# Performance work log

Measured on AMD Instinct MI355X. Metric: run time of the kernel, lower is better.

## Reference

```python
import jax, jax.numpy as jnp
import numpy as np

B, L, D, H, FF = 2, 2048, 1024, 16, 4096
DH = D // H
EPS = 1e-5  # torch LayerNorm default


def _layernorm(x, g, b):
    mu = jnp.mean(x, axis=-1, keepdims=True)
    var = jnp.mean(jnp.square(x - mu), axis=-1, keepdims=True)
    return (x - mu) * jax.lax.rsqrt(var + EPS) * g + b


def setup_inputs() -> dict:
    key = jax.random.key(0)
    ks = jax.random.split(key, 8)
    s = 0.02  # typical init scale for weights
    return {
        "x": jax.random.normal(ks[0], (B, L, D), jnp.float32),
        "pos_embed": jax.random.normal(ks[1], (1, L, D), jnp.float32) * s,
        "ln1_g": jnp.ones((D,), jnp.float32),
        "ln1_b": jnp.zeros((D,), jnp.float32),
        "Wq": jax.random.normal(ks[2], (D, D), jnp.float32) * s,
        "Wk": jax.random.normal(ks[3], (D, D), jnp.float32) * s,
        "Wv": jax.random.normal(ks[4], (D, D), jnp.float32) * s,
        "Wo": jax.random.normal(ks[5], (D, D), jnp.float32) * s,
        "bo": jnp.zeros((D,), jnp.float32),
        "ln2_g": jnp.ones((D,), jnp.float32),
        "ln2_b": jnp.zeros((D,), jnp.float32),
        "W1": jax.random.normal(ks[6], (D, FF), jnp.float32) * s,
        "b1": jnp.zeros((FF,), jnp.float32),
        "W2": jax.random.normal(ks[7], (FF, D), jnp.float32) * s,
        "b2": jnp.zeros((D,), jnp.float32),
    }


def reference(x, pos_embed, ln1_g, ln1_b, Wq, Wk, Wv, Wo, bo, ln2_g, ln2_b, W1, b1, W2, b2):
    scale = DH ** -0.5
    residual = x
    h = _layernorm(x, ln1_g, ln1_b) + pos_embed  # [B,L,D]
    # qkv projections (no bias, qkv_bias=False default), split into heads
    q = (h @ Wq).reshape(B, L, H, DH).transpose(0, 2, 1, 3)  # [B,H,L,DH]
    k = (h @ Wk).reshape(B, L, H, DH).transpose(0, 2, 1, 3)
    v = (h @ Wv).reshape(B, L, H, DH).transpose(0, 2, 1, 3)
    attn = jnp.einsum("bhqd,bhkd->bhqk", q, k) * scale  # [B,H,L,L]
    attn = jax.nn.softmax(attn, axis=-1)
    out = jnp.einsum("bhqk,bhkd->bhqd", attn, v)  # [B,H,L,DH]
    out = out.transpose(0, 2, 1, 3).reshape(B, L, D)
    out = out @ Wo + bo
    x = residual + out
    # MLP with pre-norm
    m = _layernorm(x, ln2_g, ln2_b)
    m = jax.nn.gelu(m @ W1 + b1, approximate=False) @ W2 + b2
    return x + m
```

## Files before the change

kernel.cpp:

```cpp
#include <hip/hip_runtime.h>
#include <hip/hip_bf16.h>
#include <cstdint>

typedef __bf16 bf16_t;
typedef __bf16 bf16x8 __attribute__((ext_vector_type(8)));
typedef __bf16 bf16x4v __attribute__((ext_vector_type(4)));
typedef short s16x4 __attribute__((ext_vector_type(4)));
typedef float f32x4 __attribute__((ext_vector_type(4)));

#define B_ 2
#define L_ 2048
#define D_ 1024
#define H_ 16
#define DH_ 64
#define FF_ 4096
#define M_TOT (B_*L_)

#define CLOG2 0.18033688011112042f


__device__ __forceinline__ void gload_lds16(const void* g, void* l) {
    __builtin_amdgcn_global_load_lds((__attribute__((address_space(1))) void*)g,
                                     (__attribute__((address_space(3))) void*)l,
                                     16, 0, 0);
}

__device__ __forceinline__ float fast_exp2(float v) {
    return __builtin_amdgcn_exp2f(v);
}

__device__ __forceinline__ float gelu_fast(float x) {
    float x3 = x * x * x;
    float y  = fmaf(0.044715f, x3, x);
    float e  = fast_exp2(y * 2.3022213f);
    float t  = fmaf(-2.0f, __builtin_amdgcn_rcpf(e + 1.0f), 1.0f);
    return 0.5f * x * (1.0f + t);
}

__global__ void transpose_bf16_kernel(const float* __restrict__ W, bf16_t* __restrict__ WT,
                                      int K, int N) {
    __shared__ float t[32][33];
    int tx = threadIdx.x, ty = threadIdx.y;
    int n0 = blockIdx.x * 32, k0 = blockIdx.y * 32;
#pragma unroll
    for (int i = 0; i < 4; i++)
        t[ty + 8 * i][tx] = W[(size_t)(k0 + ty + 8 * i) * N + n0 + tx];
    __syncthreads();
#pragma unroll
    for (int i = 0; i < 4; i++)
        WT[(size_t)(n0 + ty + 8 * i) * K + k0 + tx] = (bf16_t)t[tx][ty + 8 * i];
}

__global__ void transpose_qkvo_kernel(const float* __restrict__ Wq, const float* __restrict__ Wk,
                                      const float* __restrict__ Wv, const float* __restrict__ Wo,
                                      bf16_t* __restrict__ WqkvT, bf16_t* __restrict__ WoT) {
    int z = blockIdx.z;
    const float* W = (z == 0) ? Wq : (z == 1) ? Wk : (z == 2) ? Wv : Wo;
    bf16_t* dst = (z < 3) ? (WqkvT + (size_t)z * 1024 * 1024) : WoT;
    __shared__ float t[32][33];
    int tx = threadIdx.x, ty = threadIdx.y;
    int n0 = blockIdx.x * 32, k0 = blockIdx.y * 32;
#pragma unroll
    for (int i = 0; i < 4; i++)
        t[ty + 8 * i][tx] = W[(size_t)(k0 + ty + 8 * i) * D_ + n0 + tx];
    __syncthreads();
#pragma unroll
    for (int i = 0; i < 4; i++)
        dst[(size_t)(n0 + ty + 8 * i) * D_ + k0 + tx] = (bf16_t)t[tx][ty + 8 * i];
}

__global__ __launch_bounds__(256) void ln_kernel(const float* __restrict__ x,
                                                 const float* __restrict__ pos,
                                                 const float* __restrict__ g,
                                                 const float* __restrict__ beta,
                                                 bf16_t* __restrict__ out) {
    int row = blockIdx.x, tid = threadIdx.x;
    const float* xr = x + (size_t)row * D_;
    float v[4];
    float s = 0.f, sq = 0.f;
#pragma unroll
    for (int i = 0; i < 4; i++) {
        float a = xr[tid + 256 * i];
        v[i] = a; s += a; sq += a * a;
    }
#pragma unroll
    for (int o = 32; o > 0; o >>= 1) { s += __shfl_xor(s, o); sq += __shfl_xor(sq, o); }
    __shared__ float red[8];
    int wid = tid >> 6;
    if ((tid & 63) == 0) { red[wid] = s; red[4 + wid] = sq; }
    __syncthreads();
    s  = red[0] + red[1] + red[2] + red[3];
    sq = red[4] + red[5] + red[6] + red[7];
    float mu  = s * (1.f / D_);
    float var = sq * (1.f / D_) - mu * mu;
    float rs  = rsqrtf(var + 1e-5f);
    int l = row & (L_ - 1);
#pragma unroll
    for (int i = 0; i < 4; i++) {
        int c = tid + 256 * i;
        float hv = (v[i] - mu) * rs * g[c] + beta[c];
        if (pos) hv += pos[(size_t)l * D_ + c];
        out[(size_t)row * D_ + c] = (bf16_t)hv;
    }
}

__global__ __launch_bounds__(256) void ln_fuse_kernel(const float* __restrict__ x,
                                                      const float* __restrict__ bo,
                                                      const float* __restrict__ P0,
                                                      const float* __restrict__ P1,
                                                      const float* __restrict__ g,
                                                      const float* __restrict__ beta,
                                                      float* __restrict__ x2,
                                                      bf16_t* __restrict__ out) {
    int row = blockIdx.x, tid = threadIdx.x;
    size_t base = (size_t)row * D_;
    float v[4];
    float s = 0.f, sq = 0.f;
#pragma unroll
    for (int i = 0; i < 4; i++) {
        int c = tid + 256 * i;
        float a = x[base + c] + bo[c] + P0[base + c] + P1[base + c];
        v[i] = a; s += a; sq += a * a;
        x2[base + c] = a;
    }
#pragma unroll
    for (int o = 32; o > 0; o >>= 1) { s += __shfl_xor(s, o); sq += __shfl_xor(sq, o); }
    __shared__ float red[8];
    int wid = tid >> 6;
    if ((tid & 63) == 0) { red[wid] = s; red[4 + wid] = sq; }
    __syncthreads();
    s  = red[0] + red[1] + red[2] + red[3];
    sq = red[4] + red[5] + red[6] + red[7];
    float mu  = s * (1.f / D_);
    float var = sq * (1.f / D_) - mu * mu;
    float rs  = rsqrtf(var + 1e-5f);
#pragma unroll
    for (int i = 0; i < 4; i++) {
        int c = tid + 256 * i;
        out[base + c] = (bf16_t)((v[i] - mu) * rs * g[c] + beta[c]);
    }
}

__global__ __launch_bounds__(256) void reduce_out_kernel(const float* __restrict__ x2,
                                                         const float* __restrict__ bias,
                                                         const float* __restrict__ P1,
                                                         float* __restrict__ dout) {
    int i = (blockIdx.x * 256 + threadIdx.x) * 4;
    float4 a  = *(const float4*)(x2 + i);
    float4 bv = *(const float4*)(bias + (i & (D_ - 1)));
    float4 p0 = *(const float4*)(dout + i);
    float4 p1 = *(const float4*)(P1 + i);
    a.x += bv.x + p0.x + p1.x;
    a.y += bv.y + p0.y + p1.y;
    a.z += bv.z + p0.z + p1.z;
    a.w += bv.w + p0.w + p1.w;
    *(float4*)(dout + i) = a;
}

template <int EPI, typename OutT>
__global__ __launch_bounds__(256) void gemm_kernel(const bf16_t* __restrict__ A,
                                                   const bf16_t* __restrict__ BT,
                                                   OutT* __restrict__ C,
                                                   const float* __restrict__ bias,
                                                   bf16_t* __restrict__ Vt,
                                                   int M, int N, int K) {
    __shared__ __align__(16) bf16_t sA[2][128 * 32];
    __shared__ __align__(16) bf16_t sB[2][128 * 32];
    int tid = threadIdx.x;
    int lane = tid & 63, w = tid >> 6, wy = w >> 1, wx = w & 1;
    int qm = lane & 15, quad = lane >> 4;
    int row0 = blockIdx.x * 128, col0 = blockIdx.y * 128;
    f32x4 acc[4][4] = {};
    int sf[2], sra[2], scol[2];
#pragma unroll
    for (int c = 0; c < 2; c++) {
        int f = tid * 8 + c * 2048;
        sf[c] = f;
        sra[c] = f >> 5;
        int ch = (f >> 3) & 3;
        scol[c] = ((ch ^ ((sra[c] >> 1) & 3)) << 3);
    }
    int aoff[4], boff[4];
#pragma unroll
    for (int t = 0; t < 4; t++) {
        int Ra = wy * 64 + t * 16 + qm;
        int Rb = wx * 64 + t * 16 + qm;
        aoff[t] = Ra * 32 + ((quad ^ ((Ra >> 1) & 3)) << 3);
        boff[t] = Rb * 32 + ((quad ^ ((Rb >> 1) & 3)) << 3);
    }
    const bf16_t* Ab = A  + (size_t)row0 * K;
    const bf16_t* Bb = BT + (size_t)col0 * K;
#pragma unroll
    for (int c = 0; c < 2; c++) {
        gload_lds16(Ab + (size_t)sra[c] * K + scol[c], &sA[0][sf[c]]);
        gload_lds16(Bb + (size_t)sra[c] * K + scol[c], &sB[0][sf[c]]);
    }
    for (int k0 = 0; k0 < K; k0 += 32) {
        int cur = (k0 >> 5) & 1;
        __syncthreads();
        int kn = k0 + 32;
        if (kn < K) {
#pragma unroll
            for (int c = 0; c < 2; c++) {
                gload_lds16(Ab + (size_t)sra[c] * K + kn + scol[c], &sA[cur ^ 1][sf[c]]);
                gload_lds16(Bb + (size_t)sra[c] * K + kn + scol[c], &sB[cur ^ 1][sf[c]]);
            }
        }
        bf16x8 af[4], bfr[4];
#pragma unroll
        for (int mt = 0; mt < 4; mt++) af[mt] = *(const bf16x8*)&sA[cur][aoff[mt]];
#pragma unroll
        for (int nt = 0; nt < 4; nt++) bfr[nt] = *(const bf16x8*)&sB[cur][boff[nt]];
#pragma unroll
        for (int mt = 0; mt < 4; mt++)
#pragma unroll
            for (int nt = 0; nt < 4; nt++)
                acc[mt][nt] = __builtin_amdgcn_mfma_f32_16x16x32_bf16(af[mt], bfr[nt],
                                                                      acc[mt][nt], 0, 0, 0);
    }
    if (EPI == 4 && col0 >= 2048) {
#pragma unroll
        for (int mt = 0; mt < 4; mt++) {
            int row_base = row0 + wy * 64 + mt * 16 + quad * 4;
            int bb = row_base >> 11, key0 = row_base & 2047;
#pragma unroll
            for (int nt = 0; nt < 4; nt++) {
                int vcol = col0 - 2048 + wx * 64 + nt * 16 + qm;
                int hh = vcol >> 6, dd = vcol & 63;
                bf16x4v pk;
#pragma unroll
                for (int r = 0; r < 4; r++) pk[r] = (bf16_t)acc[mt][nt][r];
                *(bf16x4v*)&Vt[(size_t)(((bb << 4) + hh) * 64 + dd) * 2048 + key0] = pk;
            }
        }
        return;
    }
    float qscale = (EPI == 4 && col0 < 1024) ? CLOG2 : 1.0f;
#pragma unroll
    for (int mt = 0; mt < 4; mt++) {
#pragma unroll
        for (int nt = 0; nt < 4; nt++) {
            int col = col0 + wx * 64 + nt * 16 + qm;
#pragma unroll
            for (int r = 0; r < 4; r++) {
                int row = row0 + wy * 64 + mt * 16 + quad * 4 + r;
                float v = acc[mt][nt][r];
                if (EPI == 2) { v += bias[col]; v = gelu_fast(v); }
                if (EPI == 4) C[(size_t)row * 2048 + col] = (OutT)(v * qscale);
                else          C[(size_t)row * N + col] = (OutT)v;
            }
        }
    }
}

__global__ __launch_bounds__(256) void gemm_splitk_st_kernel(const bf16_t* __restrict__ A,
                                                             const bf16_t* __restrict__ BT,
                                                             float* __restrict__ P0,
                                                             float* __restrict__ P1,
                                                             int N, int Ktot, int Ksplit) {
    __shared__ __align__(16) bf16_t sA[2][128 * 32];
    __shared__ __align__(16) bf16_t sB[2][128 * 32];
    int tid = threadIdx.x;
    int lane = tid & 63, w = tid >> 6, wy = w >> 1, wx = w & 1;
    int qm = lane & 15, quad = lane >> 4;
    int row0 = blockIdx.x * 128, col0 = blockIdx.y * 128;
    size_t koff = (size_t)blockIdx.z * Ksplit;
    f32x4 acc[4][4] = {};
    int sf[2], sra[2], scol[2];
#pragma unroll
    for (int c = 0; c < 2; c++) {
        int f = tid * 8 + c * 2048;
        sf[c] = f;
        sra[c] = f >> 5;
        int ch = (f >> 3) & 3;
        scol[c] = ((ch ^ ((sra[c] >> 1) & 3)) << 3);
    }
    int aoff[4], boff[4];
#pragma unroll
    for (int t = 0; t < 4; t++) {
        int Ra = wy * 64 + t * 16 + qm;
        int Rb = wx * 64 + t * 16 + qm;
        aoff[t] = Ra * 32 + ((quad ^ ((Ra >> 1) & 3)) << 3);
        boff[t] = Rb * 32 + ((quad ^ ((Rb >> 1) & 3)) << 3);
    }
    const bf16_t* Ab = A  + (size_t)row0 * Ktot + koff;
    const bf16_t* Bb = BT + (size_t)col0 * Ktot + koff;
#pragma unroll
    for (int c = 0; c < 2; c++) {
        gload_lds16(Ab + (size_t)sra[c] * Ktot + scol[c], &sA[0][sf[c]]);
        gload_lds16(Bb + (size_t)sra[c] * Ktot + scol[c], &sB[0][sf[c]]);
    }
    for (int k0 = 0; k0 < Ksplit; k0 += 32) {
        int cur = (k0 >> 5) & 1;
        __syncthreads();
        int kn = k0 + 32;
        if (kn < Ksplit) {
#pragma unroll
            for (int c = 0; c < 2; c++) {
                gload_lds16(Ab + (size_t)sra[c] * Ktot + kn + scol[c], &sA[cur ^ 1][sf[c]]);
                gload_lds16(Bb + (size_t)sra[c] * Ktot + kn + scol[c], &sB[cur ^ 1][sf[c]]);
            }
        }
        bf16x8 af[4], bfr[4];
#pragma unroll
        for (int mt = 0; mt < 4; mt++) af[mt] = *(const bf16x8*)&sA[cur][aoff[mt]];
#pragma unroll
        for (int nt = 0; nt < 4; nt++) bfr[nt] = *(const bf16x8*)&sB[cur][boff[nt]];
#pragma unroll
        for (int mt = 0; mt < 4; mt++)
#pragma unroll
            for (int nt = 0; nt < 4; nt++)
                acc[mt][nt] = __builtin_amdgcn_mfma_f32_16x16x32_bf16(af[mt], bfr[nt],
                                                                      acc[mt][nt], 0, 0, 0);
    }
    float* P = blockIdx.z ? P1 : P0;
#pragma unroll
    for (int mt = 0; mt < 4; mt++) {
#pragma unroll
        for (int nt = 0; nt < 4; nt++) {
            int col = col0 + wx * 64 + nt * 16 + qm;
#pragma unroll
            for (int r = 0; r < 4; r++) {
                int row = row0 + wy * 64 + mt * 16 + quad * 4 + r;
                P[(size_t)row * N + col] = acc[mt][nt][r];
            }
        }
    }
}

__global__ __launch_bounds__(256) void attn_kernel(const bf16_t* __restrict__ QK,
                                                   const bf16_t* __restrict__ Vt,
                                                   bf16_t* __restrict__ O) {
    __shared__ __align__(16) bf16_t sK[2][64 * 64];
    __shared__ __align__(16) bf16_t sV[2][64 * 64];
    int tid = threadIdx.x, lane = tid & 63, w = tid >> 6;
    int qm = lane & 15, quad = lane >> 4;
    int q0 = blockIdx.x * 128 + w * 32;
    int bh = blockIdx.y, b = bh >> 4, h = bh & 15;

    const bf16_t* Qbase = QK + (size_t)(b * L_) * 2048 + h * 64;
    const bf16_t* Kbase = Qbase + 1024;
    const bf16_t* Vbase = Vt + (size_t)bh * 64 * 2048;

    bf16x8 qf[2][2];
#pragma unroll
    for (int g = 0; g < 2; g++) {
        const bf16_t* qp = Qbase + (size_t)(q0 + g * 16 + qm) * 2048 + quad * 8;
        qf[g][0] = *(const bf16x8*)qp;
        qf[g][1] = *(const bf16x8*)(qp + 32);
    }

    int f0 = tid * 8, f1 = f0 + 2048;
    int r0 = f0 >> 6, sc0 = ((((f0 >> 3) & 7) ^ (r0 & 7)) << 3);
    int r1 = f1 >> 6, sc1 = ((((f1 >> 3) & 7) ^ (r1 & 7)) << 3);

    gload_lds16(Kbase + (size_t)r0 * 2048 + sc0, &sK[0][f0]);
    gload_lds16(Kbase + (size_t)r1 * 2048 + sc1, &sK[0][f1]);
    gload_lds16(Vbase + (size_t)r0 * 2048 + sc0, &sV[0][f0]);
    gload_lds16(Vbase + (size_t)r1 * 2048 + sc1, &sV[0][f1]);

    f32x4 o[2][4] = {};
    float l_[2] = {0.f, 0.f};

    int kfo[4][2], vfo[4][4];
#pragma unroll
    for (int kt = 0; kt < 4; kt++) {
#pragma unroll
        for (int ks = 0; ks < 2; ks++) {
            int row = kt * 16 + qm;
            kfo[kt][ks] = row * 64 + ((((ks << 2) + quad) ^ (row & 7)) << 3);
        }
#pragma unroll
        for (int dt = 0; dt < 4; dt++) {
            int row = dt * 16 + qm;
            int cw = (kt << 1) + (quad >> 1);
            vfo[dt][kt] = row * 64 + ((cw ^ (row & 7)) << 3) + ((quad & 1) << 2);
        }
    }

    for (int kv0 = 0; kv0 < L_; kv0 += 64) {
        int cur = (kv0 >> 6) & 1;
        __syncthreads();
        int kn = kv0 + 64;
        if (kn < L_) {
            gload_lds16(Kbase + (size_t)(kn + r0) * 2048 + sc0, &sK[cur ^ 1][f0]);
            gload_lds16(Kbase + (size_t)(kn + r1) * 2048 + sc1, &sK[cur ^ 1][f1]);
            gload_lds16(Vbase + (size_t)r0 * 2048 + kn + sc0, &sV[cur ^ 1][f0]);
            gload_lds16(Vbase + (size_t)r1 * 2048 + kn + sc1, &sV[cur ^ 1][f1]);
        }

        bf16x8 kf[4][2];
#pragma unroll
        for (int kt = 0; kt < 4; kt++)
#pragma unroll
            for (int ks = 0; ks < 2; ks++)
                kf[kt][ks] = *(const bf16x8*)&sK[cur][kfo[kt][ks]];
        f32x4 s[2][4] = {};
        __builtin_amdgcn_s_setprio(1);
#pragma unroll
        for (int kt = 0; kt < 4; kt++)
#pragma unroll
            for (int ks = 0; ks < 2; ks++) {
                s[0][kt] = __builtin_amdgcn_mfma_f32_16x16x32_bf16(kf[kt][ks], qf[0][ks], s[0][kt], 0, 0, 0);
                s[1][kt] = __builtin_amdgcn_mfma_f32_16x16x32_bf16(kf[kt][ks], qf[1][ks], s[1][kt], 0, 0, 0);
            }
        __builtin_amdgcn_s_setprio(0);

        s16x4 pf[2][4];
#pragma unroll
        for (int g = 0; g < 2; g++) {
            float sum = l_[g];
#pragma unroll
            for (int kt = 0; kt < 4; kt++) {
                union { bf16x4v b; s16x4 i; } u;
#pragma unroll
                for (int r = 0; r < 4; r++) {
                    float p = fast_exp2(s[g][kt][r]);
                    sum += p;
                    u.b[r] = (bf16_t)p;
                }
                pf[g][kt] = u.i;
            }
            l_[g] = sum;
        }

        __builtin_amdgcn_s_setprio(1);
#pragma unroll
        for (int dt = 0; dt < 4; dt++)
#pragma unroll
            for (int kt = 0; kt < 4; kt++) {
                s16x4 vf = *(const s16x4*)&sV[cur][vfo[dt][kt]];
                o[0][dt] = __builtin_amdgcn_mfma_f32_16x16x16bf16_1k(vf, pf[0][kt], o[0][dt], 0, 0, 0);
                o[1][dt] = __builtin_amdgcn_mfma_f32_16x16x16bf16_1k(vf, pf[1][kt], o[1][dt], 0, 0, 0);
            }
        __builtin_amdgcn_s_setprio(0);
    }

#pragma unroll
    for (int g = 0; g < 2; g++) {
        float lt = l_[g];
        lt += __shfl_xor(lt, 16);
        lt += __shfl_xor(lt, 32);
        float rl = 1.0f / lt;
        size_t row = (size_t)(b * L_ + q0 + g * 16 + qm);
#pragma unroll
        for (int dt = 0; dt < 4; dt++) {
            bf16x4v pk;
#pragma unroll
            for (int r = 0; r < 4; r++) pk[r] = (bf16_t)(o[g][dt][r] * rl);
            *(bf16x4v*)&O[row * D_ + h * 64 + dt * 16 + quad * 4] = pk;
        }
    }
}


extern "C" void kernel_launch(void* const* d_in, const int* in_sizes, int n_in,
                              void* d_out, int out_size, void* d_ws, size_t ws_size,
                              hipStream_t stream) {
    const float* x   = (const float*)d_in[0];
    const float* pos = (const float*)d_in[1];
    const float* g1  = (const float*)d_in[2];
    const float* be1 = (const float*)d_in[3];
    const float* Wq  = (const float*)d_in[4];
    const float* Wk  = (const float*)d_in[5];
    const float* Wv  = (const float*)d_in[6];
    const float* Wo  = (const float*)d_in[7];
    const float* bo  = (const float*)d_in[8];
    const float* g2  = (const float*)d_in[9];
    const float* be2 = (const float*)d_in[10];
    const float* W1  = (const float*)d_in[11];
    const float* b1m = (const float*)d_in[12];
    const float* W2  = (const float*)d_in[13];
    const float* b2m = (const float*)d_in[14];

    char* ws = (char*)d_ws;
    const size_t MB = 1ull << 20;
    bf16_t* W2T   = (bf16_t*)(ws + 0);
    float*  x2    = (float*) (ws + 8 * MB);
    bf16_t* qk    = (bf16_t*)(ws + 24 * MB);
    bf16_t* Vt    = (bf16_t*)(ws + 40 * MB);
    bf16_t* hb    = (bf16_t*)(ws + 48 * MB);
    float*  Pwo0  = (float*) (ws + 24 * MB);
    float*  Pwo1  = (float*) (ws + 40 * MB);
    bf16_t* attnO = (bf16_t*)(ws + 56 * MB);
    bf16_t* mb    = (bf16_t*)(ws + 56 * MB);
    bf16_t* ff1   = (bf16_t*)(ws + 24 * MB);
    bf16_t* W1T   = (bf16_t*)(ws + 64 * MB);
    float*  Pff1  = (float*) (ws + 56 * MB);
    bf16_t* WqkvT = (bf16_t*)(ws + 72 * MB);
    bf16_t* WoT   = (bf16_t*)(ws + 78 * MB);

    dim3 tb(32, 8);
    transpose_qkvo_kernel<<<dim3(32, 32, 4), tb, 0, stream>>>(Wq, Wk, Wv, Wo, WqkvT, WoT);
    transpose_bf16_kernel<<<dim3(128, 32), tb, 0, stream>>>(W1, W1T, D_, FF_);
    transpose_bf16_kernel<<<dim3(32, 128), tb, 0, stream>>>(W2, W2T, FF_, D_);

    ln_kernel<<<M_TOT, 256, 0, stream>>>(x, pos, g1, be1, hb);

    gemm_kernel<4, bf16_t><<<dim3(32, 24), 256, 0, stream>>>(hb, WqkvT, qk, nullptr,
                                                             Vt, M_TOT, 3072, D_);

    attn_kernel<<<dim3(16, 32), 256, 0, stream>>>(qk, Vt, attnO);

    gemm_splitk_st_kernel<<<dim3(32, 8, 2), 256, 0, stream>>>(attnO, WoT, Pwo0, Pwo1,
                                                              D_, D_, D_ / 2);

    ln_fuse_kernel<<<M_TOT, 256, 0, stream>>>(x, bo, Pwo0, Pwo1, g2, be2, x2, mb);

    gemm_kernel<2, bf16_t><<<dim3(32, 32), 256, 0, stream>>>(mb, W1T, ff1, b1m,
                                                             nullptr, M_TOT, FF_, D_);

    gemm_splitk_st_kernel<<<dim3(32, 8, 2), 256, 0, stream>>>(ff1, W2T, (float*)d_out,
                                                              Pff1, D_, FF_, FF_ / 2);

    reduce_out_kernel<<<M_TOT * D_ / 1024, 256, 0, stream>>>(x2, b2m, Pff1, (float*)d_out);

    (void)in_sizes; (void)n_in; (void)out_size; (void)ws_size;
}
```

Measured before the change: 367.6 us.

## Widen attention KV tile to 128 and vectorize weight transpose kernels

The attention kernel now processes 128 keys per iteration instead of 64, using double-buffered LDS tiles of 128x64 for K and 64x128 for V. This halves the number of barriers and loop trips, and K fragments are loaded from LDS inline rather than hoisted into registers. Separately, the weight transpose kernels use 64x64 tiles with float4 global loads and packed bf16x4 stores, cutting the number of memory transactions. The trade-offs are more LDS per block (64KB), which may reduce occupancy, and higher register pressure from the larger score and P arrays.

```diff
diff --git a/kernel.cpp b/kernel.cpp
--- a/kernel.cpp
+++ b/kernel.cpp
@@ -39,16 +39,25 @@
 
 __global__ void transpose_bf16_kernel(const float* __restrict__ W, bf16_t* __restrict__ WT,
                                       int K, int N) {
-    __shared__ float t[32][33];
+    __shared__ float t[64][65];
     int tx = threadIdx.x, ty = threadIdx.y;
-    int n0 = blockIdx.x * 32, k0 = blockIdx.y * 32;
-#pragma unroll
-    for (int i = 0; i < 4; i++)
-        t[ty + 8 * i][tx] = W[(size_t)(k0 + ty + 8 * i) * N + n0 + tx];
+    int n0 = blockIdx.x * 64, k0 = blockIdx.y * 64;
+#pragma unroll
+    for (int i = 0; i < 4; i++) {
+        int r = ty * 4 + i;
+        float4 v = *(const float4*)(W + (size_t)(k0 + r) * N + n0 + tx * 4);
+        t[r][tx * 4 + 0] = v.x; t[r][tx * 4 + 1] = v.y;
+        t[r][tx * 4 + 2] = v.z; t[r][tx * 4 + 3] = v.w;
+    }
     __syncthreads();
 #pragma unroll
-    for (int i = 0; i < 4; i++)
-        WT[(size_t)(n0 + ty + 8 * i) * K + k0 + tx] = (bf16_t)t[tx][ty + 8 * i];
+    for (int i = 0; i < 4; i++) {
+        int r = ty * 4 + i;
+        bf16x4v pk;
+#pragma unroll
+        for (int j = 0; j < 4; j++) pk[j] = (bf16_t)t[tx * 4 + j][r];
+        *(bf16x4v*)(WT + (size_t)(n0 + r) * K + k0 + tx * 4) = pk;
+    }
 }
 
 __global__ void transpose_qkvo_kernel(const float* __restrict__ Wq, const float* __restrict__ Wk,
@@ -57,16 +66,25 @@
     int z = blockIdx.z;
     const float* W = (z == 0) ? Wq : (z == 1) ? Wk : (z == 2) ? Wv : Wo;
     bf16_t* dst = (z < 3) ? (WqkvT + (size_t)z * 1024 * 1024) : WoT;
-    __shared__ float t[32][33];
+    __shared__ float t[64][65];
     int tx = threadIdx.x, ty = threadIdx.y;
-    int n0 = blockIdx.x * 32, k0 = blockIdx.y * 32;
-#pragma unroll
-    for (int i = 0; i < 4; i++)
-        t[ty + 8 * i][tx] = W[(size_t)(k0 + ty + 8 * i) * D_ + n0 + tx];
+    int n0 = blockIdx.x * 64, k0 = blockIdx.y * 64;
+#pragma unroll
+    for (int i = 0; i < 4; i++) {
+        int r = ty * 4 + i;
+        float4 v = *(const float4*)(W + (size_t)(k0 + r) * D_ + n0 + tx * 4);
+        t[r][tx * 4 + 0] = v.x; t[r][tx * 4 + 1] = v.y;
+        t[r][tx * 4 + 2] = v.z; t[r][tx * 4 + 3] = v.w;
+    }
     __syncthreads();
 #pragma unroll
-    for (int i = 0; i < 4; i++)
-        dst[(size_t)(n0 + ty + 8 * i) * D_ + k0 + tx] = (bf16_t)t[tx][ty + 8 * i];
+    for (int i = 0; i < 4; i++) {
+        int r = ty * 4 + i;
+        bf16x4v pk;
+#pragma unroll
+        for (int j = 0; j < 4; j++) pk[j] = (bf16_t)t[tx * 4 + j][r];
+        *(bf16x4v*)(dst + (size_t)(n0 + r) * D_ + k0 + tx * 4) = pk;
+    }
 }
 
 __global__ __launch_bounds__(256) void ln_kernel(const float* __restrict__ x,
@@ -331,8 +349,8 @@
 __global__ __launch_bounds__(256) void attn_kernel(const bf16_t* __restrict__ QK,
                                                    const bf16_t* __restrict__ Vt,
                                                    bf16_t* __restrict__ O) {
-    __shared__ __align__(16) bf16_t sK[2][64 * 64];
-    __shared__ __align__(16) bf16_t sV[2][64 * 64];
+    __shared__ __align__(16) bf16_t sK[2][128 * 64];
+    __shared__ __align__(16) bf16_t sV[2][64 * 128];
     int tid = threadIdx.x, lane = tid & 63, w = tid >> 6;
     int qm = lane & 15, quad = lane >> 4;
     int q0 = blockIdx.x * 128 + w * 32;
@@ -350,68 +368,71 @@
         qf[g][1] = *(const bf16x8*)(qp + 32);
     }
 
-    int f0 = tid * 8, f1 = f0 + 2048;
-    int r0 = f0 >> 6, sc0 = ((((f0 >> 3) & 7) ^ (r0 & 7)) << 3);
-    int r1 = f1 >> 6, sc1 = ((((f1 >> 3) & 7) ^ (r1 & 7)) << 3);
-
-    gload_lds16(Kbase + (size_t)r0 * 2048 + sc0, &sK[0][f0]);
-    gload_lds16(Kbase + (size_t)r1 * 2048 + sc1, &sK[0][f1]);
-    gload_lds16(Vbase + (size_t)r0 * 2048 + sc0, &sV[0][f0]);
-    gload_lds16(Vbase + (size_t)r1 * 2048 + sc1, &sV[0][f1]);
+    int ksf[4], ksr[4], ksc[4], vsf[4], vsr[4], vsc[4];
+#pragma unroll
+    for (int c = 0; c < 4; c++) {
+        int f = tid * 8 + c * 2048;
+        ksf[c] = f;
+        ksr[c] = f >> 6;
+        ksc[c] = ((((f >> 3) & 7) ^ (ksr[c] & 7)) << 3);
+        vsf[c] = f;
+        vsr[c] = f >> 7;
+        vsc[c] = ((((f >> 3) & 15) ^ (vsr[c] & 7)) << 3);
+    }
+#pragma unroll
+    for (int c = 0; c < 4; c++) {
+        gload_lds16(Kbase + (size_t)ksr[c] * 2048 + ksc[c], &sK[0][ksf[c]]);
+        gload_lds16(Vbase + (size_t)vsr[c] * 2048 + vsc[c], &sV[0][vsf[c]]);
+    }
 
     f32x4 o[2][4] = {};
     float l_[2] = {0.f, 0.f};
 
-    int kfo[4][2], vfo[4][4];
-#pragma unroll
-    for (int kt = 0; kt < 4; kt++) {
-#pragma unroll
-        for (int ks = 0; ks < 2; ks++) {
-            int row = kt * 16 + qm;
+    int kfo[8][2], vfo[4][8];
+#pragma unroll
+    for (int kt = 0; kt < 8; kt++) {
+        int row = kt * 16 + qm;
+#pragma unroll
+        for (int ks = 0; ks < 2; ks++)
             kfo[kt][ks] = row * 64 + ((((ks << 2) + quad) ^ (row & 7)) << 3);
-        }
 #pragma unroll
         for (int dt = 0; dt < 4; dt++) {
-            int row = dt * 16 + qm;
+            int vrow = dt * 16 + qm;
             int cw = (kt << 1) + (quad >> 1);
-            vfo[dt][kt] = row * 64 + ((cw ^ (row & 7)) << 3) + ((quad & 1) << 2);
-        }
-    }
-
-    for (int kv0 = 0; kv0 < L_; kv0 += 64) {
-        int cur = (kv0 >> 6) & 1;
+            vfo[dt][kt] = vrow * 128 + ((cw ^ (vrow & 7)) << 3) + ((quad & 1) << 2);
+        }
+    }
+
+    for (int kv0 = 0; kv0 < L_; kv0 += 128) {
+        int cur = (kv0 >> 7) & 1;
         __syncthreads();
-        int kn = kv0 + 64;
+        int kn = kv0 + 128;
         if (kn < L_) {
-            gload_lds16(Kbase + (size_t)(kn + r0) * 2048 + sc0, &sK[cur ^ 1][f0]);
-            gload_lds16(Kbase + (size_t)(kn + r1) * 2048 + sc1, &sK[cur ^ 1][f1]);
-            gload_lds16(Vbase + (size_t)r0 * 2048 + kn + sc0, &sV[cur ^ 1][f0]);
-            gload_lds16(Vbase + (size_t)r1 * 2048 + kn + sc1, &sV[cur ^ 1][f1]);
-        }
-
-        bf16x8 kf[4][2];
-#pragma unroll
-        for (int kt = 0; kt < 4; kt++)
-#pragma unroll
-            for (int ks = 0; ks < 2; ks++)
-                kf[kt][ks] = *(const bf16x8*)&sK[cur][kfo[kt][ks]];
-        f32x4 s[2][4] = {};
+#pragma unroll
+            for (int c = 0; c < 4; c++) {
+                gload_lds16(Kbase + (size_t)(kn + ksr[c]) * 2048 + ksc[c], &sK[cur ^ 1][ksf[c]]);
+                gload_lds16(Vbase + (size_t)vsr[c] * 2048 + kn + vsc[c], &sV[cur ^ 1][vsf[c]]);
+            }
+        }
+
+        f32x4 s[2][8] = {};
         __builtin_amdgcn_s_setprio(1);
 #pragma unroll
-        for (int kt = 0; kt < 4; kt++)
+        for (int kt = 0; kt < 8; kt++)
 #pragma unroll
             for (int ks = 0; ks < 2; ks++) {
-                s[0][kt] = __builtin_amdgcn_mfma_f32_16x16x32_bf16(kf[kt][ks], qf[0][ks], s[0][kt], 0, 0, 0);
-                s[1][kt] = __builtin_amdgcn_mfma_f32_16x16x32_bf16(kf[kt][ks], qf[1][ks], s[1][kt], 0, 0, 0);
+                bf16x8 kf = *(const bf16x8*)&sK[cur][kfo[kt][ks]];
+                s[0][kt] = __builtin_amdgcn_mfma_f32_16x16x32_bf16(kf, qf[0][ks], s[0][kt], 0, 0, 0);
+                s[1][kt] = __builtin_amdgcn_mfma_f32_16x16x32_bf16(kf, qf[1][ks], s[1][kt], 0, 0, 0);
             }
         __builtin_amdgcn_s_setprio(0);
 
-        s16x4 pf[2][4];
+        s16x4 pf[2][8];
 #pragma unroll
         for (int g = 0; g < 2; g++) {
             float sum = l_[g];
 #pragma unroll
-            for (int kt = 0; kt < 4; kt++) {
+            for (int kt = 0; kt < 8; kt++) {
                 union { bf16x4v b; s16x4 i; } u;
 #pragma unroll
                 for (int r = 0; r < 4; r++) {
@@ -428,7 +449,7 @@
 #pragma unroll
         for (int dt = 0; dt < 4; dt++)
 #pragma unroll
-            for (int kt = 0; kt < 4; kt++) {
+            for (int kt = 0; kt < 8; kt++) {
                 s16x4 vf = *(const s16x4*)&sV[cur][vfo[dt][kt]];
                 o[0][dt] = __builtin_amdgcn_mfma_f32_16x16x16bf16_1k(vf, pf[0][kt], o[0][dt], 0, 0, 0);
                 o[1][dt] = __builtin_amdgcn_mfma_f32_16x16x16bf16_1k(vf, pf[1][kt], o[1][dt], 0, 0, 0);
@@ -490,10 +511,10 @@
     bf16_t* WqkvT = (bf16_t*)(ws + 72 * MB);
     bf16_t* WoT   = (bf16_t*)(ws + 78 * MB);
 
-    dim3 tb(32, 8);
-    transpose_qkvo_kernel<<<dim3(32, 32, 4), tb, 0, stream>>>(Wq, Wk, Wv, Wo, WqkvT, WoT);
-    transpose_bf16_kernel<<<dim3(128, 32), tb, 0, stream>>>(W1, W1T, D_, FF_);
-    transpose_bf16_kernel<<<dim3(32, 128), tb, 0, stream>>>(W2, W2T, FF_, D_);
+    dim3 tt(16, 16);
+    transpose_qkvo_kernel<<<dim3(16, 16, 4), tt, 0, stream>>>(Wq, Wk, Wv, Wo, WqkvT, WoT);
+    transpose_bf16_kernel<<<dim3(64, 16), tt, 0, stream>>>(W1, W1T, D_, FF_);
+    transpose_bf16_kernel<<<dim3(16, 64), tt, 0, stream>>>(W2, W2T, FF_, D_);
 
     ln_kernel<<<M_TOT, 256, 0, stream>>>(x, pos, g1, be1, hb);
 
```

Result: no change. 370.8 us (+0.9%).

## Use 256x256-tile 512-thread GEMM for FF1 and vectorize weight transposes

Applied to the files above, without the earlier changes.

Replaces the 128x128 FF1 GEMM (bias+GELU epilogue) with a new 256x256-tile kernel using 8 waves, each computing 128x64, with double-buffered LDS loaded via global_load_lds. This raises arithmetic intensity per tile and cuts global traffic, but the grid shrinks to 256 blocks and per-thread register pressure rises. The weight transpose kernels also move to 64x64 tiles with float4 loads and packed bf16x4 stores to cut per-element memory transactions.

```diff
diff --git a/kernel.cpp b/kernel.cpp
--- a/kernel.cpp
+++ b/kernel.cpp
@@ -39,16 +39,25 @@
 
 __global__ void transpose_bf16_kernel(const float* __restrict__ W, bf16_t* __restrict__ WT,
                                       int K, int N) {
-    __shared__ float t[32][33];
+    __shared__ float t[64][65];
     int tx = threadIdx.x, ty = threadIdx.y;
-    int n0 = blockIdx.x * 32, k0 = blockIdx.y * 32;
-#pragma unroll
-    for (int i = 0; i < 4; i++)
-        t[ty + 8 * i][tx] = W[(size_t)(k0 + ty + 8 * i) * N + n0 + tx];
+    int n0 = blockIdx.x * 64, k0 = blockIdx.y * 64;
+#pragma unroll
+    for (int i = 0; i < 4; i++) {
+        int r = ty * 4 + i;
+        float4 v = *(const float4*)(W + (size_t)(k0 + r) * N + n0 + tx * 4);
+        t[r][tx * 4 + 0] = v.x; t[r][tx * 4 + 1] = v.y;
+        t[r][tx * 4 + 2] = v.z; t[r][tx * 4 + 3] = v.w;
+    }
     __syncthreads();
 #pragma unroll
-    for (int i = 0; i < 4; i++)
-        WT[(size_t)(n0 + ty + 8 * i) * K + k0 + tx] = (bf16_t)t[tx][ty + 8 * i];
+    for (int i = 0; i < 4; i++) {
+        int r = ty * 4 + i;
+        bf16x4v pk;
+#pragma unroll
+        for (int j = 0; j < 4; j++) pk[j] = (bf16_t)t[tx * 4 + j][r];
+        *(bf16x4v*)(WT + (size_t)(n0 + r) * K + k0 + tx * 4) = pk;
+    }
 }
 
 __global__ void transpose_qkvo_kernel(const float* __restrict__ Wq, const float* __restrict__ Wk,
@@ -57,16 +66,25 @@
     int z = blockIdx.z;
     const float* W = (z == 0) ? Wq : (z == 1) ? Wk : (z == 2) ? Wv : Wo;
     bf16_t* dst = (z < 3) ? (WqkvT + (size_t)z * 1024 * 1024) : WoT;
-    __shared__ float t[32][33];
+    __shared__ float t[64][65];
     int tx = threadIdx.x, ty = threadIdx.y;
-    int n0 = blockIdx.x * 32, k0 = blockIdx.y * 32;
-#pragma unroll
-    for (int i = 0; i < 4; i++)
-        t[ty + 8 * i][tx] = W[(size_t)(k0 + ty + 8 * i) * D_ + n0 + tx];
+    int n0 = blockIdx.x * 64, k0 = blockIdx.y * 64;
+#pragma unroll
+    for (int i = 0; i < 4; i++) {
+        int r = ty * 4 + i;
+        float4 v = *(const float4*)(W + (size_t)(k0 + r) * D_ + n0 + tx * 4);
+        t[r][tx * 4 + 0] = v.x; t[r][tx * 4 + 1] = v.y;
+        t[r][tx * 4 + 2] = v.z; t[r][tx * 4 + 3] = v.w;
+    }
     __syncthreads();
 #pragma unroll
-    for (int i = 0; i < 4; i++)
-        dst[(size_t)(n0 + ty + 8 * i) * D_ + k0 + tx] = (bf16_t)t[tx][ty + 8 * i];
+    for (int i = 0; i < 4; i++) {
+        int r = ty * 4 + i;
+        bf16x4v pk;
+#pragma unroll
+        for (int j = 0; j < 4; j++) pk[j] = (bf16_t)t[tx * 4 + j][r];
+        *(bf16x4v*)(dst + (size_t)(n0 + r) * D_ + k0 + tx * 4) = pk;
+    }
 }
 
 __global__ __launch_bounds__(256) void ln_kernel(const float* __restrict__ x,
@@ -248,6 +266,83 @@
                 if (EPI == 2) { v += bias[col]; v = gelu_fast(v); }
                 if (EPI == 4) C[(size_t)row * 2048 + col] = (OutT)(v * qscale);
                 else          C[(size_t)row * N + col] = (OutT)v;
+            }
+        }
+    }
+}
+
+__global__ __launch_bounds__(512, 2) void gemm256_gelu_kernel(const bf16_t* __restrict__ A,
+                                                              const bf16_t* __restrict__ BT,
+                                                              bf16_t* __restrict__ C,
+                                                              const float* __restrict__ bias,
+                                                              int N, int K) {
+    __shared__ __align__(16) bf16_t sA[2][256 * 32];
+    __shared__ __align__(16) bf16_t sB[2][256 * 32];
+    int tid = threadIdx.x;
+    int lane = tid & 63, w = tid >> 6, wy = w >> 2, wx = w & 3;
+    int qm = lane & 15, quad = lane >> 4;
+    int row0 = blockIdx.x * 256, col0 = blockIdx.y * 256;
+    f32x4 acc[8][4] = {};
+    int sf[2], sra[2], scol[2];
+#pragma unroll
+    for (int c = 0; c < 2; c++) {
+        int f = tid * 8 + c * 4096;
+        sf[c] = f;
+        sra[c] = f >> 5;
+        int ch = (f >> 3) & 3;
+        scol[c] = ((ch ^ ((sra[c] >> 1) & 3)) << 3);
+    }
+    int aoff[8], boff[4];
+#pragma unroll
+    for (int t = 0; t < 8; t++) {
+        int Ra = wy * 128 + t * 16 + qm;
+        aoff[t] = Ra * 32 + ((quad ^ ((Ra >> 1) & 3)) << 3);
+    }
+#pragma unroll
+    for (int t = 0; t < 4; t++) {
+        int Rb = wx * 64 + t * 16 + qm;
+        boff[t] = Rb * 32 + ((quad ^ ((Rb >> 1) & 3)) << 3);
+    }
+    const bf16_t* Ab = A  + (size_t)row0 * K;
+    const bf16_t* Bb = BT + (size_t)col0 * K;
+#pragma unroll
+    for (int c = 0; c < 2; c++) {
+        gload_lds16(Ab + (size_t)sra[c] * K + scol[c], &sA[0][sf[c]]);
+        gload_lds16(Bb + (size_t)sra[c] * K + scol[c], &sB[0][sf[c]]);
+    }
+    for (int k0 = 0; k0 < K; k0 += 32) {
+        int cur = (k0 >> 5) & 1;
+        __syncthreads();
+        int kn = k0 + 32;
+        if (kn < K) {
+#pragma unroll
+            for (int c = 0; c < 2; c++) {
+                gload_lds16(Ab + (size_t)sra[c] * K + kn + scol[c], &sA[cur ^ 1][sf[c]]);
+                gload_lds16(Bb + (size_t)sra[c] * K + kn + scol[c], &sB[cur ^ 1][sf[c]]);
+            }
+        }
+        bf16x8 bfr[4];
+#pragma unroll
+        for (int nt = 0; nt < 4; nt++) bfr[nt] = *(const bf16x8*)&sB[cur][boff[nt]];
+#pragma unroll
+        for (int mt = 0; mt < 8; mt++) {
+            bf16x8 af = *(const bf16x8*)&sA[cur][aoff[mt]];
+#pragma unroll
+            for (int nt = 0; nt < 4; nt++)
+                acc[mt][nt] = __builtin_amdgcn_mfma_f32_16x16x32_bf16(af, bfr[nt],
+                                                                      acc[mt][nt], 0, 0, 0);
+        }
+    }
+#pragma unroll
+    for (int mt = 0; mt < 8; mt++) {
+#pragma unroll
+        for (int nt = 0; nt < 4; nt++) {
+            int col = col0 + wx * 64 + nt * 16 + qm;
+            float bv = bias[col];
+#pragma unroll
+            for (int r = 0; r < 4; r++) {
+                int row = row0 + wy * 128 + mt * 16 + quad * 4 + r;
+                C[(size_t)row * N + col] = (bf16_t)gelu_fast(acc[mt][nt][r] + bv);
             }
         }
     }
@@ -490,10 +585,10 @@
     bf16_t* WqkvT = (bf16_t*)(ws + 72 * MB);
     bf16_t* WoT   = (bf16_t*)(ws + 78 * MB);
 
-    dim3 tb(32, 8);
-    transpose_qkvo_kernel<<<dim3(32, 32, 4), tb, 0, stream>>>(Wq, Wk, Wv, Wo, WqkvT, WoT);
-    transpose_bf16_kernel<<<dim3(128, 32), tb, 0, stream>>>(W1, W1T, D_, FF_);
-    transpose_bf16_kernel<<<dim3(32, 128), tb, 0, stream>>>(W2, W2T, FF_, D_);
+    dim3 tt(16, 16);
+    transpose_qkvo_kernel<<<dim3(16, 16, 4), tt, 0, stream>>>(Wq, Wk, Wv, Wo, WqkvT, WoT);
+    transpose_bf16_kernel<<<dim3(64, 16), tt, 0, stream>>>(W1, W1T, D_, FF_);
+    transpose_bf16_kernel<<<dim3(16, 64), tt, 0, stream>>>(W2, W2T, FF_, D_);
 
     ln_kernel<<<M_TOT, 256, 0, stream>>>(x, pos, g1, be1, hb);
 
@@ -507,8 +602,7 @@
 
     ln_fuse_kernel<<<M_TOT, 256, 0, stream>>>(x, bo, Pwo0, Pwo1, g2, be2, x2, mb);
 
-    gemm_kernel<2, bf16_t><<<dim3(32, 32), 256, 0, stream>>>(mb, W1T, ff1, b1m,
-                                                             nullptr, M_TOT, FF_, D_);
+    gemm256_gelu_kernel<<<dim3(16, 16), 512, 0, stream>>>(mb, W1T, ff1, b1m, FF_, D_);
 
     gemm_splitk_st_kernel<<<dim3(32, 8, 2), 256, 0, stream>>>(ff1, W2T, (float*)d_out,
                                                               Pff1, D_, FF_, FF_ / 2);
```

Measured after the change: 365.3 us. Within noise of the previous version (-0.6%).
